# Kernel optimization log

Hardware: AMD Instinct MI355X
Metric: run time of the kernel (lower is better)

## Reference

```python
import jax, jax.numpy as jnp
import numpy as np

B, S, C = 64, 512, 512   # batch, subseq_length, in_features
H, D = 4, 128            # n_heads, hidden_features (H*D == C)
LN_EPS = 1e-5


def setup_inputs() -> dict:
    key = jax.random.key(0)
    k_h, k_w, k_b = jax.random.split(key, 3)
    h = jax.random.normal(k_h, (B, S, C), dtype=jnp.float32)
    # stacked per-head Linear weights, stored as [H, in, hid] for x @ W
    W = jax.random.normal(k_w, (H, C, D), dtype=jnp.float32) * (1.0 / np.sqrt(C))
    b = jax.random.normal(k_b, (H, D), dtype=jnp.float32) * 0.01
    adj = jnp.ones((S, S), dtype=jnp.float32)
    gamma = jnp.ones((C,), dtype=jnp.float32)
    beta = jnp.zeros((C,), dtype=jnp.float32)
    return {"t": 0, "h": h, "W": W, "b": b, "adj": adj, "gamma": gamma, "beta": beta}


def reference(t, h, W, b, adj, gamma, beta):
    # per-head projection: [H, B, S, D]
    hp = jnp.einsum("bsc,hcd->hbsd", h, W) + b[:, None, None, :]
    # raw scores, multiplicative adjacency mask (non-standard: mask BEFORE softmax by multiply)
    scores = jnp.einsum("hbsd,hbtd->hbst", hp, hp) * adj
    attn = jax.nn.softmax(scores, axis=-1)
    out = jnp.einsum("hbst,hbtd->hbsd", attn, hp)
    # concat heads along feature dim -> [B, S, H*D] == [B, S, C]
    out = jnp.transpose(out, (1, 2, 0, 3)).reshape(h.shape[0], h.shape[1], -1)
    # LayerNorm over last dim
    mu = jnp.mean(out, axis=-1, keepdims=True)
    var = jnp.mean(jnp.square(out - mu), axis=-1, keepdims=True)
    out = (out - mu) * jax.lax.rsqrt(var + LN_EPS) * gamma + beta
    # GELU (exact erf form, matching torch nn.GELU default)
    return jax.nn.gelu(out, approximate=False)
```

## Files before the change

kernel.cpp:

```cpp
#include <hip/hip_runtime.h>
#include <stdint.h>


typedef float  f32x4   __attribute__((ext_vector_type(4)));
typedef short  bf16x8  __attribute__((ext_vector_type(8)));
typedef unsigned short ushort8 __attribute__((ext_vector_type(8)));
typedef unsigned int   uint2v  __attribute__((ext_vector_type(2)));

#define GLD16(src, dst)                                                        \
  __builtin_amdgcn_global_load_lds(                                            \
      (const __attribute__((address_space(1))) void*)(src),                    \
      (__attribute__((address_space(3))) void*)(dst), 16, 0, 0)

__device__ __forceinline__ unsigned short f32_to_bf16(float x) {
  union { float f; unsigned int u; } v; v.f = x;
  unsigned int r = v.u + 0x7FFFu + ((v.u >> 16) & 1u);
  return (unsigned short)(r >> 16);
}
__device__ __forceinline__ float bf16_to_f32(unsigned int h) {
  union { float f; unsigned int u; } v; v.u = h << 16;
  return v.f;
}
__device__ __forceinline__ f32x4 mfma16(bf16x8 a, bf16x8 b, f32x4 c) {
  return __builtin_amdgcn_mfma_f32_16x16x32_bf16(a, b, c, 0, 0, 0);
}
__device__ __forceinline__ float bperm_f(int srcLane, float v) {
  return __int_as_float(__builtin_amdgcn_ds_bpermute(srcLane << 2, __float_as_int(v)));
}
__device__ __forceinline__ uint2v tr_read(const unsigned short* p) {
  uint2v r;
  asm volatile("ds_read_b64_tr_b16 %0, %1"
               : "=v"(r)
               : "v"((const __attribute__((address_space(3))) void*)p)
               : "memory");
  return r;
}

__global__ __launch_bounds__(256) void cast_split_h(
    const float* __restrict__ src, unsigned short* __restrict__ dhi,
    unsigned short* __restrict__ dlo) {
  size_t i = ((size_t)blockIdx.x * 256 + threadIdx.x) * 8;
  f32x4 a = *(const f32x4*)(src + i);
  f32x4 b = *(const f32x4*)(src + i + 4);
  ushort8 hi, lo;
#pragma unroll
  for (int e = 0; e < 4; ++e) {
    unsigned short h0 = f32_to_bf16(a[e]);
    hi[e] = h0; lo[e] = f32_to_bf16(a[e] - bf16_to_f32(h0));
    unsigned short h1 = f32_to_bf16(b[e]);
    hi[4 + e] = h1; lo[4 + e] = f32_to_bf16(b[e] - bf16_to_f32(h1));
  }
  *(ushort8*)(dhi + i) = hi;
  *(ushort8*)(dlo + i) = lo;
}

__global__ __launch_bounds__(256) void cast_split_Wt(
    const float* __restrict__ W, unsigned short* __restrict__ whi,
    unsigned short* __restrict__ wlo) {
  int o = blockIdx.x * 256 + threadIdx.x;
  int hd = o >> 16;
  int rem = o & 65535;
  int d = rem >> 9;
  int c = rem & 511;
  float v = W[((size_t)(hd * 512 + c)) * 128 + d];
  unsigned short h0 = f32_to_bf16(v);
  whi[o] = h0;
  wlo[o] = f32_to_bf16(v - bf16_to_f32(h0));
}

__global__ __launch_bounds__(256) void cast_adj(
    const float* __restrict__ src, unsigned short* __restrict__ dst) {
  size_t i = ((size_t)blockIdx.x * 256 + threadIdx.x) * 8;
  f32x4 a = *(const f32x4*)(src + i);
  f32x4 b = *(const f32x4*)(src + i + 4);
  ushort8 o;
#pragma unroll
  for (int e = 0; e < 4; ++e) {
    o[e] = f32_to_bf16(a[e]);
    o[4 + e] = f32_to_bf16(b[e]);
  }
  *(ushort8*)(dst + i) = o;
}

__global__ __launch_bounds__(256, 2) void proj_gemm(
    const unsigned short* __restrict__ ahi, const unsigned short* __restrict__ alo,
    const unsigned short* __restrict__ whi, const unsigned short* __restrict__ wlo,
    const float* __restrict__ bias, unsigned short* __restrict__ hp_hi,
    unsigned short* __restrict__ hp_lo) {
  int bid = blockIdx.x;
  int swz = (bid & 7) * 128 + (bid >> 3);
  int nt = swz & 3, mt = swz >> 2;
  int m0 = mt * 128, n0 = nt * 128;

  __shared__ alignas(16) unsigned short Ah[128 * 32], Al[128 * 32];
  __shared__ alignas(16) unsigned short Bh[128 * 32], Bl[128 * 32];

  int tid = threadIdx.x, wv = tid >> 6, lane = tid & 63;
  int l15 = lane & 15, l4 = lane >> 4;
  int wr = wv >> 1, wc = wv & 1;

  f32x4 acc[4][4];
#pragma unroll
  for (int a = 0; a < 4; ++a)
#pragma unroll
    for (int b = 0; b < 4; ++b) acc[a][b] = (f32x4){0.f, 0.f, 0.f, 0.f};

  for (int ks = 0; ks < 16; ++ks) {
    int k0 = ks * 32;
    for (int i = wv; i < 32; i += 4) {
      int grp = i >> 3, j = i & 7;
      int row = j * 16 + (lane >> 2);
      int off = (lane & 3) * 16;
      int sw = ((row >> 1) & 3) << 4;
      const unsigned short* sb;
      unsigned short* db;
      size_t srcoff;
      if (grp == 0)      { sb = ahi; db = Ah; srcoff = ((size_t)(m0 + row) * 512 + k0) * 2; }
      else if (grp == 1) { sb = alo; db = Al; srcoff = ((size_t)(m0 + row) * 512 + k0) * 2; }
      else if (grp == 2) { sb = whi; db = Bh; srcoff = ((size_t)(nt * 128 + row) * 512 + k0) * 2; }
      else               { sb = wlo; db = Bl; srcoff = ((size_t)(nt * 128 + row) * 512 + k0) * 2; }
      GLD16((const char*)sb + srcoff + (off ^ sw), db + j * 512);
    }
    __syncthreads();

    bf16x8 fah[4], fal[4], fbh[4], fbl[4];
#pragma unroll
    for (int f = 0; f < 4; ++f) {
      int mr = wr * 64 + f * 16 + l15;
      int aadr = mr * 64 + ((16 * l4) ^ (((mr >> 1) & 3) << 4));
      fah[f] = *(const bf16x8*)((const char*)Ah + aadr);
      fal[f] = *(const bf16x8*)((const char*)Al + aadr);
      int nr = wc * 64 + f * 16 + l15;
      int badr = nr * 64 + ((16 * l4) ^ (((nr >> 1) & 3) << 4));
      fbh[f] = *(const bf16x8*)((const char*)Bh + badr);
      fbl[f] = *(const bf16x8*)((const char*)Bl + badr);
    }
#pragma unroll
    for (int a = 0; a < 4; ++a)
#pragma unroll
      for (int b = 0; b < 4; ++b) {
        acc[a][b] = mfma16(fah[a], fbh[b], acc[a][b]);
        acc[a][b] = mfma16(fah[a], fbl[b], acc[a][b]);
        acc[a][b] = mfma16(fal[a], fbh[b], acc[a][b]);
      }
    __syncthreads();
  }

#pragma unroll
  for (int a = 0; a < 4; ++a) {
    __syncthreads();
#pragma unroll
    for (int b = 0; b < 4; ++b) {
      int cloc = wc * 64 + b * 16 + l15;
      float bv = bias[n0 + cloc];
#pragma unroll
      for (int r = 0; r < 4; ++r) {
        int rloc = wr * 16 + 4 * l4 + r;
        float v = acc[a][b][r] + bv;
        unsigned short hh = f32_to_bf16(v);
        Ah[rloc * 128 + cloc] = hh;
        Al[rloc * 128 + cloc] = f32_to_bf16(v - bf16_to_f32(hh));
      }
    }
    __syncthreads();
    int rr = tid >> 3, c16 = (tid & 7) * 16;
    int mg = m0 + (rr >> 4) * 64 + a * 16 + (rr & 15);
    bf16x8 vh0 = *(const bf16x8*)(Ah + rr * 128 + c16);
    bf16x8 vh1 = *(const bf16x8*)(Ah + rr * 128 + c16 + 8);
    bf16x8 vl0 = *(const bf16x8*)(Al + rr * 128 + c16);
    bf16x8 vl1 = *(const bf16x8*)(Al + rr * 128 + c16 + 8);
    *(bf16x8*)(hp_hi + (size_t)mg * 512 + n0 + c16) = vh0;
    *(bf16x8*)(hp_hi + (size_t)mg * 512 + n0 + c16 + 8) = vh1;
    *(bf16x8*)(hp_lo + (size_t)mg * 512 + n0 + c16) = vl0;
    *(bf16x8*)(hp_lo + (size_t)mg * 512 + n0 + c16 + 8) = vl1;
  }
}

__global__ __launch_bounds__(256, 3) void attn_kernel(
    const unsigned short* __restrict__ hp_hi, const unsigned short* __restrict__ hp_lo,
    const unsigned short* __restrict__ adjb, float* __restrict__ out) {
  int bid = blockIdx.x;
  int swz = (bid & 7) * 256 + (bid >> 3);
  int qt = swz & 7;
  int hd = (swz >> 3) & 3;
  int bb = swz >> 5;
  int q0 = qt * 64;

  __shared__ alignas(16) unsigned short SM[24576];

  int tid = threadIdx.x, w = tid >> 6, lane = tid & 63;
  int l15 = lane & 15, l4 = lane >> 4;
  int qg = q0 + w * 16 + l15;

  bf16x8 qh[4], ql[4];
  {
    size_t base = ((size_t)bb * 512 + qg) * 512 + hd * 128 + 8 * l4;
#pragma unroll
    for (int ds = 0; ds < 4; ++ds) {
      qh[ds] = *(const bf16x8*)(hp_hi + base + ds * 32);
      ql[ds] = *(const bf16x8*)(hp_lo + base + ds * 32);
    }
  }

  f32x4 o[8];
#pragma unroll
  for (int vf = 0; vf < 8; ++vf) o[vf] = (f32x4){0.f, 0.f, 0.f, 0.f};
  float m_run = -3.0e38f, l_run = 0.f;

  const unsigned short* ssb = (w & 2) ? hp_lo : hp_hi;
  int sdst = (w & 2) ? 4096 : 0;
  int sdbase = (w & 1) * 4;
  int skv = lane >> 1, sdh = lane & 1;

  {
    size_t rowb = ((size_t)(bb * 512 + skv)) * 1024 + hd * 256 + sdh * 16;
#pragma unroll
    for (int s2 = 0; s2 < 4; ++s2) {
      int sd = sdbase + s2;
      GLD16((const char*)ssb + rowb + sd * 32, SM + sdst + sd * 512);
    }
  }
  asm volatile("s_waitcnt vmcnt(0)" ::: "memory");
  __syncthreads();

  for (int t = 0; t < 16; ++t) {
    int kv0 = t * 32;
    const unsigned short* Kb = SM + ((t & 1) << 13);
    const unsigned short* Khi = Kb;
    const unsigned short* Klo = Kb + 4096;

    if (t < 15) {
      unsigned short* Nb = SM + (((t + 1) & 1) << 13) + sdst;
      size_t rowb = ((size_t)(bb * 512 + kv0 + 32 + skv)) * 1024 + hd * 256 + sdh * 16;
#pragma unroll
      for (int s2 = 0; s2 < 4; ++s2) {
        int sd = sdbase + s2;
        GLD16((const char*)ssb + rowb + sd * 32, Nb + sd * 512);
      }
    }
    uint2 ua0 = *(const uint2*)(adjb + (size_t)qg * 512 + kv0 + 4 * l4);
    uint2 ua1 = *(const uint2*)(adjb + (size_t)qg * 512 + kv0 + 16 + 4 * l4);
    f32x4 av0, av1;
    av0[0] = bf16_to_f32(ua0.x & 0xFFFFu); av0[1] = bf16_to_f32(ua0.x >> 16);
    av0[2] = bf16_to_f32(ua0.y & 0xFFFFu); av0[3] = bf16_to_f32(ua0.y >> 16);
    av1[0] = bf16_to_f32(ua1.x & 0xFFFFu); av1[1] = bf16_to_f32(ua1.x >> 16);
    av1[2] = bf16_to_f32(ua1.y & 0xFFFFu); av1[3] = bf16_to_f32(ua1.y >> 16);

    f32x4 sc0 = {0.f, 0.f, 0.f, 0.f}, sc1 = {0.f, 0.f, 0.f, 0.f};
#pragma unroll
    for (int ds = 0; ds < 4; ++ds) {
      int boff = (2 * ds + (l4 >> 1)) * 1024 + 16 * (l4 & 1);
      int a0 = boff + l15 * 32;
      int a1 = boff + (16 + l15) * 32;
      bf16x8 kh0 = *(const bf16x8*)((const char*)Khi + a0);
      bf16x8 kl0 = *(const bf16x8*)((const char*)Klo + a0);
      bf16x8 kh1 = *(const bf16x8*)((const char*)Khi + a1);
      bf16x8 kl1 = *(const bf16x8*)((const char*)Klo + a1);
      sc0 = mfma16(kh0, qh[ds], sc0); sc1 = mfma16(kh1, qh[ds], sc1);
      sc0 = mfma16(kh0, ql[ds], sc0); sc1 = mfma16(kh1, ql[ds], sc1);
      sc0 = mfma16(kl0, qh[ds], sc0); sc1 = mfma16(kl1, qh[ds], sc1);
    }

    float p0[4], p1[4];
    float tm = -3.0e38f;
#pragma unroll
    for (int r = 0; r < 4; ++r) {
      p0[r] = sc0[r] * av0[r];
      p1[r] = sc1[r] * av1[r];
      tm = fmaxf(tm, fmaxf(p0[r], p1[r]));
    }
    tm = fmaxf(tm, __shfl_xor(tm, 16));
    tm = fmaxf(tm, __shfl_xor(tm, 32));
    if (__any(tm > m_run + 8.0f)) {
      float mn = fmaxf(m_run, tm);
      float scl = __expf(m_run - mn);
      m_run = mn;
      l_run *= scl;
      f32x4 s4;
#pragma unroll
      for (int r = 0; r < 4; ++r) s4[r] = bperm_f(4 * l4 + r, scl);
#pragma unroll
      for (int vf = 0; vf < 8; ++vf)
#pragma unroll
        for (int r = 0; r < 4; ++r) o[vf][r] *= s4[r];
    }
    float ps = 0.f;
#pragma unroll
    for (int r = 0; r < 4; ++r) {
      p0[r] = __expf(p0[r] - m_run); ps += p0[r];
      p1[r] = __expf(p1[r] - m_run); ps += p1[r];
    }
    ps += __shfl_xor(ps, 16);
    ps += __shfl_xor(ps, 32);
    l_run += ps;

    union PU { bf16x8 v; unsigned u[4]; } pah;
#pragma unroll
    for (int i = 0; i < 4; ++i) {
      float fa = (i < 2) ? p0[2 * i] : p1[2 * (i - 2)];
      float fb = (i < 2) ? p0[2 * i + 1] : p1[2 * (i - 2) + 1];
      pah.u[i] = (__float_as_uint(fa) >> 16) |
                 (__float_as_uint(fb) & 0xFFFF0000u);
    }

    const unsigned short* trb = Khi + lane * 4;
    union VU { bf16x8 v; uint2v u2[2]; } vh[8];
#pragma unroll
    for (int vf = 0; vf < 8; ++vf) {
      vh[vf].u2[0] = tr_read(trb + vf * 512);
      vh[vf].u2[1] = tr_read(trb + vf * 512 + 256);
    }
    asm volatile("s_waitcnt lgkmcnt(0)" ::: "memory");
    __builtin_amdgcn_sched_barrier(0);
#pragma unroll
    for (int vf = 0; vf < 8; ++vf)
      o[vf] = mfma16(pah.v, vh[vf].v, o[vf]);
    asm volatile("s_waitcnt vmcnt(0) lgkmcnt(0)" ::: "memory");
    __syncthreads();
  }

  float rinv = 1.0f / l_run;
  f32x4 r4;
#pragma unroll
  for (int r = 0; r < 4; ++r) r4[r] = bperm_f(4 * l4 + r, rinv);
  float* wbase = (float*)SM + w * 2048;
#pragma unroll
  for (int vf = 0; vf < 8; ++vf)
#pragma unroll
    for (int r = 0; r < 4; ++r)
      wbase[(4 * l4 + r) * 128 + vf * 16 + l15] = o[vf][r] * r4[r];
  __syncthreads();
#pragma unroll
  for (int p = 0; p < 4; ++p) {
    int row = p * 4 + l4;
    f32x4 v0 = *(const f32x4*)(wbase + row * 128 + l15 * 8);
    f32x4 v1 = *(const f32x4*)(wbase + row * 128 + l15 * 8 + 4);
    size_t mg = (size_t)bb * 512 + q0 + w * 16 + row;
    float* op = out + mg * 512 + hd * 128 + l15 * 8;
    *(f32x4*)op = v0;
    *(f32x4*)(op + 4) = v1;
  }
}

__global__ __launch_bounds__(256) void ln_gelu_kernel(
    float* __restrict__ io, const float* __restrict__ gamma,
    const float* __restrict__ beta) {
  int w = threadIdx.x >> 6, lane = threadIdx.x & 63;
  size_t row = (size_t)blockIdx.x * 4 + w;
  float* p = io + row * 512;
  f32x4 x0 = *(const f32x4*)(p + lane * 8);
  f32x4 x1 = *(const f32x4*)(p + lane * 8 + 4);
  float s = x0[0] + x0[1] + x0[2] + x0[3] + x1[0] + x1[1] + x1[2] + x1[3];
#pragma unroll
  for (int off = 32; off >= 1; off >>= 1) s += __shfl_xor(s, off);
  float mu = s * (1.0f / 512.0f);
  float vs = 0.f;
#pragma unroll
  for (int e = 0; e < 4; ++e) {
    float d0 = x0[e] - mu; vs += d0 * d0;
    float d1 = x1[e] - mu; vs += d1 * d1;
  }
#pragma unroll
  for (int off = 32; off >= 1; off >>= 1) vs += __shfl_xor(vs, off);
  float rs = rsqrtf(vs * (1.0f / 512.0f) + 1e-5f);
  f32x4 g0 = *(const f32x4*)(gamma + lane * 8);
  f32x4 g1 = *(const f32x4*)(gamma + lane * 8 + 4);
  f32x4 b0 = *(const f32x4*)(beta + lane * 8);
  f32x4 b1 = *(const f32x4*)(beta + lane * 8 + 4);
  f32x4 y0, y1;
#pragma unroll
  for (int e = 0; e < 4; ++e) {
    float y = (x0[e] - mu) * rs * g0[e] + b0[e];
    y0[e] = 0.5f * y * (1.0f + erff(y * 0.70710678118654752f));
    float z = (x1[e] - mu) * rs * g1[e] + b1[e];
    y1[e] = 0.5f * z * (1.0f + erff(z * 0.70710678118654752f));
  }
  *(f32x4*)(p + lane * 8) = y0;
  *(f32x4*)(p + lane * 8 + 4) = y1;
}

extern "C" void kernel_launch(void* const* d_in, const int* in_sizes, int n_in,
                              void* d_out, int out_size, void* d_ws, size_t ws_size,
                              hipStream_t stream) {
  const float* h     = (const float*)d_in[1];
  const float* W     = (const float*)d_in[2];
  const float* bias  = (const float*)d_in[3];
  const float* adj   = (const float*)d_in[4];
  const float* gamma = (const float*)d_in[5];
  const float* beta  = (const float*)d_in[6];
  float* out = (float*)d_out;

  unsigned short* ws = (unsigned short*)d_ws;
  unsigned short* h_hi   = ws;
  unsigned short* h_lo   = ws + 16777216;
  unsigned short* hp_hi  = ws + 33554432;
  unsigned short* hp_lo  = ws + 50331648;
  unsigned short* Wt_hi  = ws + 67108864;
  unsigned short* Wt_lo  = ws + 67371008;
  unsigned short* adj_bf = ws;

  cast_split_h<<<8192, 256, 0, stream>>>(h, h_hi, h_lo);
  cast_split_Wt<<<1024, 256, 0, stream>>>(W, Wt_hi, Wt_lo);
  proj_gemm<<<1024, 256, 0, stream>>>(h_hi, h_lo, Wt_hi, Wt_lo, bias, hp_hi, hp_lo);
  cast_adj<<<128, 256, 0, stream>>>(adj, adj_bf);
  attn_kernel<<<2048, 256, 0, stream>>>(hp_hi, hp_lo, adj_bf, out);
  ln_gelu_kernel<<<8192, 256, 0, stream>>>(out, gamma, beta);
}
```

Baseline: 211.7 us.

## Process two query fragments per wave in attention kernel with 128-thread blocks

Each attention block now runs two waves instead of four, and each wave handles 32 query rows as two 16-row fragments. The K/V tile loaded from shared memory is reused across both fragments, halving LDS reads per MFMA. Each wave now loads twice as much of the K tile into LDS, and the output staging uses a padded 132-float stride. The cost is higher register pressure (doubled accumulators and Q fragments) and fewer waves per block, which may reduce latency hiding.

```diff
diff --git a/kernel.cpp b/kernel.cpp
--- a/kernel.cpp
+++ b/kernel.cpp
@@ -176,7 +176,7 @@
   }
 }
 
-__global__ __launch_bounds__(256, 3) void attn_kernel(
+__global__ __launch_bounds__(128, 2) void attn_kernel(
     const unsigned short* __restrict__ hp_hi, const unsigned short* __restrict__ hp_lo,
     const unsigned short* __restrict__ adjb, float* __restrict__ out) {
   int bid = blockIdx.x;
@@ -186,39 +186,40 @@
   int bb = swz >> 5;
   int q0 = qt * 64;
 
-  __shared__ alignas(16) unsigned short SM[24576];
+  __shared__ alignas(16) unsigned short SM[26624];
 
   int tid = threadIdx.x, w = tid >> 6, lane = tid & 63;
   int l15 = lane & 15, l4 = lane >> 4;
-  int qg = q0 + w * 16 + l15;
-
-  bf16x8 qh[4], ql[4];
-  {
-    size_t base = ((size_t)bb * 512 + qg) * 512 + hd * 128 + 8 * l4;
+  int qgb = q0 + w * 32 + l15;
+
+  bf16x8 qh[2][4], ql[2][4];
+#pragma unroll
+  for (int nf = 0; nf < 2; ++nf) {
+    size_t base = ((size_t)bb * 512 + qgb + nf * 16) * 512 + hd * 128 + 8 * l4;
 #pragma unroll
     for (int ds = 0; ds < 4; ++ds) {
-      qh[ds] = *(const bf16x8*)(hp_hi + base + ds * 32);
-      ql[ds] = *(const bf16x8*)(hp_lo + base + ds * 32);
-    }
-  }
-
-  f32x4 o[8];
-#pragma unroll
-  for (int vf = 0; vf < 8; ++vf) o[vf] = (f32x4){0.f, 0.f, 0.f, 0.f};
-  float m_run = -3.0e38f, l_run = 0.f;
-
-  const unsigned short* ssb = (w & 2) ? hp_lo : hp_hi;
-  int sdst = (w & 2) ? 4096 : 0;
-  int sdbase = (w & 1) * 4;
+      qh[nf][ds] = *(const bf16x8*)(hp_hi + base + ds * 32);
+      ql[nf][ds] = *(const bf16x8*)(hp_lo + base + ds * 32);
+    }
+  }
+
+  f32x4 o[2][8];
+#pragma unroll
+  for (int nf = 0; nf < 2; ++nf)
+#pragma unroll
+    for (int vf = 0; vf < 8; ++vf) o[nf][vf] = (f32x4){0.f, 0.f, 0.f, 0.f};
+  float m_run[2] = {-3.0e38f, -3.0e38f};
+  float l_run[2] = {0.f, 0.f};
+
+  const unsigned short* ssb = w ? hp_lo : hp_hi;
+  int sdst = w ? 4096 : 0;
   int skv = lane >> 1, sdh = lane & 1;
 
   {
     size_t rowb = ((size_t)(bb * 512 + skv)) * 1024 + hd * 256 + sdh * 16;
 #pragma unroll
-    for (int s2 = 0; s2 < 4; ++s2) {
-      int sd = sdbase + s2;
+    for (int sd = 0; sd < 8; ++sd)
       GLD16((const char*)ssb + rowb + sd * 32, SM + sdst + sd * 512);
-    }
   }
   asm volatile("s_waitcnt vmcnt(0)" ::: "memory");
   __syncthreads();
@@ -233,20 +234,22 @@
       unsigned short* Nb = SM + (((t + 1) & 1) << 13) + sdst;
       size_t rowb = ((size_t)(bb * 512 + kv0 + 32 + skv)) * 1024 + hd * 256 + sdh * 16;
 #pragma unroll
-      for (int s2 = 0; s2 < 4; ++s2) {
-        int sd = sdbase + s2;
+      for (int sd = 0; sd < 8; ++sd)
         GLD16((const char*)ssb + rowb + sd * 32, Nb + sd * 512);
-      }
-    }
-    uint2 ua0 = *(const uint2*)(adjb + (size_t)qg * 512 + kv0 + 4 * l4);
-    uint2 ua1 = *(const uint2*)(adjb + (size_t)qg * 512 + kv0 + 16 + 4 * l4);
-    f32x4 av0, av1;
-    av0[0] = bf16_to_f32(ua0.x & 0xFFFFu); av0[1] = bf16_to_f32(ua0.x >> 16);
-    av0[2] = bf16_to_f32(ua0.y & 0xFFFFu); av0[3] = bf16_to_f32(ua0.y >> 16);
-    av1[0] = bf16_to_f32(ua1.x & 0xFFFFu); av1[1] = bf16_to_f32(ua1.x >> 16);
-    av1[2] = bf16_to_f32(ua1.y & 0xFFFFu); av1[3] = bf16_to_f32(ua1.y >> 16);
-
-    f32x4 sc0 = {0.f, 0.f, 0.f, 0.f}, sc1 = {0.f, 0.f, 0.f, 0.f};
+    }
+    uint2 ua[2][2];
+#pragma unroll
+    for (int nf = 0; nf < 2; ++nf) {
+      const unsigned short* ab = adjb + (size_t)(qgb + nf * 16) * 512 + kv0;
+      ua[nf][0] = *(const uint2*)(ab + 4 * l4);
+      ua[nf][1] = *(const uint2*)(ab + 16 + 4 * l4);
+    }
+
+    f32x4 sc[2][2];
+#pragma unroll
+    for (int nf = 0; nf < 2; ++nf)
+#pragma unroll
+      for (int mf = 0; mf < 2; ++mf) sc[nf][mf] = (f32x4){0.f, 0.f, 0.f, 0.f};
 #pragma unroll
     for (int ds = 0; ds < 4; ++ds) {
       int boff = (2 * ds + (l4 >> 1)) * 1024 + 16 * (l4 & 1);
@@ -256,51 +259,68 @@
       bf16x8 kl0 = *(const bf16x8*)((const char*)Klo + a0);
       bf16x8 kh1 = *(const bf16x8*)((const char*)Khi + a1);
       bf16x8 kl1 = *(const bf16x8*)((const char*)Klo + a1);
-      sc0 = mfma16(kh0, qh[ds], sc0); sc1 = mfma16(kh1, qh[ds], sc1);
-      sc0 = mfma16(kh0, ql[ds], sc0); sc1 = mfma16(kh1, ql[ds], sc1);
-      sc0 = mfma16(kl0, qh[ds], sc0); sc1 = mfma16(kl1, qh[ds], sc1);
-    }
-
-    float p0[4], p1[4];
-    float tm = -3.0e38f;
-#pragma unroll
-    for (int r = 0; r < 4; ++r) {
-      p0[r] = sc0[r] * av0[r];
-      p1[r] = sc1[r] * av1[r];
-      tm = fmaxf(tm, fmaxf(p0[r], p1[r]));
-    }
-    tm = fmaxf(tm, __shfl_xor(tm, 16));
-    tm = fmaxf(tm, __shfl_xor(tm, 32));
-    if (__any(tm > m_run + 8.0f)) {
-      float mn = fmaxf(m_run, tm);
-      float scl = __expf(m_run - mn);
-      m_run = mn;
-      l_run *= scl;
-      f32x4 s4;
-#pragma unroll
-      for (int r = 0; r < 4; ++r) s4[r] = bperm_f(4 * l4 + r, scl);
-#pragma unroll
-      for (int vf = 0; vf < 8; ++vf)
-#pragma unroll
-        for (int r = 0; r < 4; ++r) o[vf][r] *= s4[r];
-    }
-    float ps = 0.f;
-#pragma unroll
-    for (int r = 0; r < 4; ++r) {
-      p0[r] = __expf(p0[r] - m_run); ps += p0[r];
-      p1[r] = __expf(p1[r] - m_run); ps += p1[r];
-    }
-    ps += __shfl_xor(ps, 16);
-    ps += __shfl_xor(ps, 32);
-    l_run += ps;
-
-    union PU { bf16x8 v; unsigned u[4]; } pah;
-#pragma unroll
-    for (int i = 0; i < 4; ++i) {
-      float fa = (i < 2) ? p0[2 * i] : p1[2 * (i - 2)];
-      float fb = (i < 2) ? p0[2 * i + 1] : p1[2 * (i - 2) + 1];
-      pah.u[i] = (__float_as_uint(fa) >> 16) |
-                 (__float_as_uint(fb) & 0xFFFF0000u);
+#pragma unroll
+      for (int nf = 0; nf < 2; ++nf) {
+        sc[nf][0] = mfma16(kh0, qh[nf][ds], sc[nf][0]);
+        sc[nf][1] = mfma16(kh1, qh[nf][ds], sc[nf][1]);
+        sc[nf][0] = mfma16(kh0, ql[nf][ds], sc[nf][0]);
+        sc[nf][1] = mfma16(kh1, ql[nf][ds], sc[nf][1]);
+        sc[nf][0] = mfma16(kl0, qh[nf][ds], sc[nf][0]);
+        sc[nf][1] = mfma16(kl1, qh[nf][ds], sc[nf][1]);
+      }
+    }
+
+    union PU { bf16x8 v; unsigned u[4]; } pah[2];
+#pragma unroll
+    for (int nf = 0; nf < 2; ++nf) {
+      f32x4 av0, av1;
+      av0[0] = bf16_to_f32(ua[nf][0].x & 0xFFFFu);
+      av0[1] = bf16_to_f32(ua[nf][0].x >> 16);
+      av0[2] = bf16_to_f32(ua[nf][0].y & 0xFFFFu);
+      av0[3] = bf16_to_f32(ua[nf][0].y >> 16);
+      av1[0] = bf16_to_f32(ua[nf][1].x & 0xFFFFu);
+      av1[1] = bf16_to_f32(ua[nf][1].x >> 16);
+      av1[2] = bf16_to_f32(ua[nf][1].y & 0xFFFFu);
+      av1[3] = bf16_to_f32(ua[nf][1].y >> 16);
+      float p0[4], p1[4];
+      float tm = -3.0e38f;
+#pragma unroll
+      for (int r = 0; r < 4; ++r) {
+        p0[r] = sc[nf][0][r] * av0[r];
+        p1[r] = sc[nf][1][r] * av1[r];
+        tm = fmaxf(tm, fmaxf(p0[r], p1[r]));
+      }
+      tm = fmaxf(tm, __shfl_xor(tm, 16));
+      tm = fmaxf(tm, __shfl_xor(tm, 32));
+      if (__any(tm > m_run[nf] + 8.0f)) {
+        float mn = fmaxf(m_run[nf], tm);
+        float scl = __expf(m_run[nf] - mn);
+        m_run[nf] = mn;
+        l_run[nf] *= scl;
+        f32x4 s4;
+#pragma unroll
+        for (int r = 0; r < 4; ++r) s4[r] = bperm_f(4 * l4 + r, scl);
+#pragma unroll
+        for (int vf = 0; vf < 8; ++vf)
+#pragma unroll
+          for (int r = 0; r < 4; ++r) o[nf][vf][r] *= s4[r];
+      }
+      float ps = 0.f;
+#pragma unroll
+      for (int r = 0; r < 4; ++r) {
+        p0[r] = __expf(p0[r] - m_run[nf]); ps += p0[r];
+        p1[r] = __expf(p1[r] - m_run[nf]); ps += p1[r];
+      }
+      ps += __shfl_xor(ps, 16);
+      ps += __shfl_xor(ps, 32);
+      l_run[nf] += ps;
+#pragma unroll
+      for (int i = 0; i < 4; ++i) {
+        float fa = (i < 2) ? p0[2 * i] : p1[2 * (i - 2)];
+        float fb = (i < 2) ? p0[2 * i + 1] : p1[2 * (i - 2) + 1];
+        pah[nf].u[i] = (__float_as_uint(fa) >> 16) |
+                       (__float_as_uint(fb) & 0xFFFF0000u);
+      }
     }
 
     const unsigned short* trb = Khi + lane * 4;
@@ -313,30 +333,40 @@
     asm volatile("s_waitcnt lgkmcnt(0)" ::: "memory");
     __builtin_amdgcn_sched_barrier(0);
 #pragma unroll
-    for (int vf = 0; vf < 8; ++vf)
-      o[vf] = mfma16(pah.v, vh[vf].v, o[vf]);
+    for (int vf = 0; vf < 8; ++vf) {
+      o[0][vf] = mfma16(pah[0].v, vh[vf].v, o[0][vf]);
+      o[1][vf] = mfma16(pah[1].v, vh[vf].v, o[1][vf]);
+    }
     asm volatile("s_waitcnt vmcnt(0) lgkmcnt(0)" ::: "memory");
     __syncthreads();
   }
 
-  float rinv = 1.0f / l_run;
-  f32x4 r4;
-#pragma unroll
-  for (int r = 0; r < 4; ++r) r4[r] = bperm_f(4 * l4 + r, rinv);
-  float* wbase = (float*)SM + w * 2048;
+  float rinv0 = 1.0f / l_run[0];
+  float rinv1 = 1.0f / l_run[1];
+  f32x4 r40, r41;
+#pragma unroll
+  for (int r = 0; r < 4; ++r) {
+    r40[r] = bperm_f(4 * l4 + r, rinv0);
+    r41[r] = bperm_f(4 * l4 + r, rinv1);
+  }
+  float* wb = (float*)SM;
 #pragma unroll
   for (int vf = 0; vf < 8; ++vf)
 #pragma unroll
-    for (int r = 0; r < 4; ++r)
-      wbase[(4 * l4 + r) * 128 + vf * 16 + l15] = o[vf][r] * r4[r];
+    for (int r = 0; r < 4; ++r) {
+      int c = vf * 16 + l15;
+      wb[(w * 32 + 4 * l4 + r) * 132 + c]      = o[0][vf][r] * r40[r];
+      wb[(w * 32 + 16 + 4 * l4 + r) * 132 + c] = o[1][vf][r] * r41[r];
+    }
   __syncthreads();
 #pragma unroll
-  for (int p = 0; p < 4; ++p) {
-    int row = p * 4 + l4;
-    f32x4 v0 = *(const f32x4*)(wbase + row * 128 + l15 * 8);
-    f32x4 v1 = *(const f32x4*)(wbase + row * 128 + l15 * 8 + 4);
-    size_t mg = (size_t)bb * 512 + q0 + w * 16 + row;
-    float* op = out + mg * 512 + hd * 128 + l15 * 8;
+  for (int p = 0; p < 8; ++p) {
+    int row = p * 8 + (tid >> 4);
+    int col = (tid & 15) * 8;
+    f32x4 v0 = *(const f32x4*)(wb + row * 132 + col);
+    f32x4 v1 = *(const f32x4*)(wb + row * 132 + col + 4);
+    size_t mg = (size_t)bb * 512 + q0 + row;
+    float* op = out + mg * 512 + hd * 128 + col;
     *(f32x4*)op = v0;
     *(f32x4*)(op + 4) = v1;
   }
@@ -403,6 +433,6 @@
   cast_split_Wt<<<1024, 256, 0, stream>>>(W, Wt_hi, Wt_lo);
   proj_gemm<<<1024, 256, 0, stream>>>(h_hi, h_lo, Wt_hi, Wt_lo, bias, hp_hi, hp_lo);
   cast_adj<<<128, 256, 0, stream>>>(adj, adj_bf);
-  attn_kernel<<<2048, 256, 0, stream>>>(hp_hi, hp_lo, adj_bf, out);
+  attn_kernel<<<2048, 128, 0, stream>>>(hp_hi, hp_lo, adj_bf, out);
   ln_gelu_kernel<<<8192, 256, 0, stream>>>(out, gamma, beta);
 }
```

Measured after the change: 232.1 us. 1.1x slower.

## Double-buffer projection GEMM loads and store attention output as bf16

Applied to the files above, without the earlier changes.

The projection GEMM now uses a two-stage LDS buffer. The next K-slice is prefetched with global_load_lds while MFMAs run on the current slice, which hides global load latency behind compute. Separately, the attention kernel writes its output as bf16 to a workspace buffer instead of fp32, and the LayerNorm+GELU kernel reads bf16 and writes fp32 to the final output. This halves the intermediate traffic at some precision cost before LayerNorm. The doubled LDS (64KB) may lower GEMM occupancy.

```diff
diff --git a/kernel.cpp b/kernel.cpp
--- a/kernel.cpp
+++ b/kernel.cpp
@@ -92,8 +92,7 @@
   int nt = swz & 3, mt = swz >> 2;
   int m0 = mt * 128, n0 = nt * 128;
 
-  __shared__ alignas(16) unsigned short Ah[128 * 32], Al[128 * 32];
-  __shared__ alignas(16) unsigned short Bh[128 * 32], Bl[128 * 32];
+  __shared__ alignas(16) unsigned short PSM[32768];
 
   int tid = threadIdx.x, wv = tid >> 6, lane = tid & 63;
   int l15 = lane & 15, l4 = lane >> 4;
@@ -105,24 +104,42 @@
 #pragma unroll
     for (int b = 0; b < 4; ++b) acc[a][b] = (f32x4){0.f, 0.f, 0.f, 0.f};
 
+  for (int i = wv; i < 32; i += 4) {
+    int grp = i >> 3, j = i & 7;
+    int row = j * 16 + (lane >> 2);
+    int off = (lane & 3) * 16;
+    int sw = ((row >> 1) & 3) << 4;
+    const unsigned short* sb = (grp == 0) ? ahi : (grp == 1) ? alo
+                             : (grp == 2) ? whi : wlo;
+    size_t srcoff = (grp < 2) ? ((size_t)(m0 + row) * 512) * 2
+                              : ((size_t)(nt * 128 + row) * 512) * 2;
+    GLD16((const char*)sb + srcoff + (off ^ sw), PSM + grp * 4096 + j * 512);
+  }
+  asm volatile("s_waitcnt vmcnt(0)" ::: "memory");
+  __syncthreads();
+
   for (int ks = 0; ks < 16; ++ks) {
-    int k0 = ks * 32;
-    for (int i = wv; i < 32; i += 4) {
-      int grp = i >> 3, j = i & 7;
-      int row = j * 16 + (lane >> 2);
-      int off = (lane & 3) * 16;
-      int sw = ((row >> 1) & 3) << 4;
-      const unsigned short* sb;
-      unsigned short* db;
-      size_t srcoff;
-      if (grp == 0)      { sb = ahi; db = Ah; srcoff = ((size_t)(m0 + row) * 512 + k0) * 2; }
-      else if (grp == 1) { sb = alo; db = Al; srcoff = ((size_t)(m0 + row) * 512 + k0) * 2; }
-      else if (grp == 2) { sb = whi; db = Bh; srcoff = ((size_t)(nt * 128 + row) * 512 + k0) * 2; }
-      else               { sb = wlo; db = Bl; srcoff = ((size_t)(nt * 128 + row) * 512 + k0) * 2; }
-      GLD16((const char*)sb + srcoff + (off ^ sw), db + j * 512);
-    }
-    __syncthreads();
-
+    const unsigned short* base = PSM + (ks & 1) * 16384;
+    if (ks < 15) {
+      unsigned short* nb = PSM + ((ks + 1) & 1) * 16384;
+      int k1 = (ks + 1) * 32;
+      for (int i = wv; i < 32; i += 4) {
+        int grp = i >> 3, j = i & 7;
+        int row = j * 16 + (lane >> 2);
+        int off = (lane & 3) * 16;
+        int sw = ((row >> 1) & 3) << 4;
+        const unsigned short* sb = (grp == 0) ? ahi : (grp == 1) ? alo
+                                 : (grp == 2) ? whi : wlo;
+        size_t srcoff = (grp < 2) ? ((size_t)(m0 + row) * 512 + k1) * 2
+                                  : ((size_t)(nt * 128 + row) * 512 + k1) * 2;
+        GLD16((const char*)sb + srcoff + (off ^ sw), nb + grp * 4096 + j * 512);
+      }
+    }
+
+    const unsigned short* Ah = base;
+    const unsigned short* Al = base + 4096;
+    const unsigned short* Bh = base + 8192;
+    const unsigned short* Bl = base + 12288;
     bf16x8 fah[4], fal[4], fbh[4], fbl[4];
 #pragma unroll
     for (int f = 0; f < 4; ++f) {
@@ -143,9 +160,12 @@
         acc[a][b] = mfma16(fah[a], fbl[b], acc[a][b]);
         acc[a][b] = mfma16(fal[a], fbh[b], acc[a][b]);
       }
+    asm volatile("s_waitcnt vmcnt(0) lgkmcnt(0)" ::: "memory");
     __syncthreads();
   }
 
+  unsigned short* Eh = PSM;
+  unsigned short* El = PSM + 4096;
 #pragma unroll
   for (int a = 0; a < 4; ++a) {
     __syncthreads();
@@ -158,17 +178,17 @@
         int rloc = wr * 16 + 4 * l4 + r;
         float v = acc[a][b][r] + bv;
         unsigned short hh = f32_to_bf16(v);
-        Ah[rloc * 128 + cloc] = hh;
-        Al[rloc * 128 + cloc] = f32_to_bf16(v - bf16_to_f32(hh));
+        Eh[rloc * 128 + cloc] = hh;
+        El[rloc * 128 + cloc] = f32_to_bf16(v - bf16_to_f32(hh));
       }
     }
     __syncthreads();
     int rr = tid >> 3, c16 = (tid & 7) * 16;
     int mg = m0 + (rr >> 4) * 64 + a * 16 + (rr & 15);
-    bf16x8 vh0 = *(const bf16x8*)(Ah + rr * 128 + c16);
-    bf16x8 vh1 = *(const bf16x8*)(Ah + rr * 128 + c16 + 8);
-    bf16x8 vl0 = *(const bf16x8*)(Al + rr * 128 + c16);
-    bf16x8 vl1 = *(const bf16x8*)(Al + rr * 128 + c16 + 8);
+    bf16x8 vh0 = *(const bf16x8*)(Eh + rr * 128 + c16);
+    bf16x8 vh1 = *(const bf16x8*)(Eh + rr * 128 + c16 + 8);
+    bf16x8 vl0 = *(const bf16x8*)(El + rr * 128 + c16);
+    bf16x8 vl1 = *(const bf16x8*)(El + rr * 128 + c16 + 8);
     *(bf16x8*)(hp_hi + (size_t)mg * 512 + n0 + c16) = vh0;
     *(bf16x8*)(hp_hi + (size_t)mg * 512 + n0 + c16 + 8) = vh1;
     *(bf16x8*)(hp_lo + (size_t)mg * 512 + n0 + c16) = vl0;
@@ -178,7 +198,7 @@
 
 __global__ __launch_bounds__(256, 3) void attn_kernel(
     const unsigned short* __restrict__ hp_hi, const unsigned short* __restrict__ hp_lo,
-    const unsigned short* __restrict__ adjb, float* __restrict__ out) {
+    const unsigned short* __restrict__ adjb, unsigned short* __restrict__ ob) {
   int bid = blockIdx.x;
   int swz = (bid & 7) * 256 + (bid >> 3);
   int qt = swz & 7;
@@ -335,30 +355,36 @@
     int row = p * 4 + l4;
     f32x4 v0 = *(const f32x4*)(wbase + row * 128 + l15 * 8);
     f32x4 v1 = *(const f32x4*)(wbase + row * 128 + l15 * 8 + 4);
+    ushort8 o8;
+#pragma unroll
+    for (int e = 0; e < 4; ++e) {
+      o8[e] = f32_to_bf16(v0[e]);
+      o8[4 + e] = f32_to_bf16(v1[e]);
+    }
     size_t mg = (size_t)bb * 512 + q0 + w * 16 + row;
-    float* op = out + mg * 512 + hd * 128 + l15 * 8;
-    *(f32x4*)op = v0;
-    *(f32x4*)(op + 4) = v1;
+    *(ushort8*)(ob + mg * 512 + hd * 128 + l15 * 8) = o8;
   }
 }
 
 __global__ __launch_bounds__(256) void ln_gelu_kernel(
-    float* __restrict__ io, const float* __restrict__ gamma,
-    const float* __restrict__ beta) {
+    const unsigned short* __restrict__ in, float* __restrict__ outp,
+    const float* __restrict__ gamma, const float* __restrict__ beta) {
   int w = threadIdx.x >> 6, lane = threadIdx.x & 63;
   size_t row = (size_t)blockIdx.x * 4 + w;
-  float* p = io + row * 512;
-  f32x4 x0 = *(const f32x4*)(p + lane * 8);
-  f32x4 x1 = *(const f32x4*)(p + lane * 8 + 4);
-  float s = x0[0] + x0[1] + x0[2] + x0[3] + x1[0] + x1[1] + x1[2] + x1[3];
+  ushort8 v = *(const ushort8*)(in + row * 512 + lane * 8);
+  float x[8];
+#pragma unroll
+  for (int e = 0; e < 8; ++e) x[e] = bf16_to_f32((unsigned int)(unsigned short)v[e]);
+  float s = 0.f;
+#pragma unroll
+  for (int e = 0; e < 8; ++e) s += x[e];
 #pragma unroll
   for (int off = 32; off >= 1; off >>= 1) s += __shfl_xor(s, off);
   float mu = s * (1.0f / 512.0f);
   float vs = 0.f;
 #pragma unroll
-  for (int e = 0; e < 4; ++e) {
-    float d0 = x0[e] - mu; vs += d0 * d0;
-    float d1 = x1[e] - mu; vs += d1 * d1;
+  for (int e = 0; e < 8; ++e) {
+    float d = x[e] - mu; vs += d * d;
   }
 #pragma unroll
   for (int off = 32; off >= 1; off >>= 1) vs += __shfl_xor(vs, off);
@@ -370,13 +396,14 @@
   f32x4 y0, y1;
 #pragma unroll
   for (int e = 0; e < 4; ++e) {
-    float y = (x0[e] - mu) * rs * g0[e] + b0[e];
+    float y = (x[e] - mu) * rs * g0[e] + b0[e];
     y0[e] = 0.5f * y * (1.0f + erff(y * 0.70710678118654752f));
-    float z = (x1[e] - mu) * rs * g1[e] + b1[e];
+    float z = (x[4 + e] - mu) * rs * g1[e] + b1[e];
     y1[e] = 0.5f * z * (1.0f + erff(z * 0.70710678118654752f));
   }
-  *(f32x4*)(p + lane * 8) = y0;
-  *(f32x4*)(p + lane * 8 + 4) = y1;
+  float* p = outp + row * 512 + lane * 8;
+  *(f32x4*)p = y0;
+  *(f32x4*)(p + 4) = y1;
 }
 
 extern "C" void kernel_launch(void* const* d_in, const int* in_sizes, int n_in,
@@ -398,11 +425,12 @@
   unsigned short* Wt_hi  = ws + 67108864;
   unsigned short* Wt_lo  = ws + 67371008;
   unsigned short* adj_bf = ws;
+  unsigned short* ob     = ws + 16777216;
 
   cast_split_h<<<8192, 256, 0, stream>>>(h, h_hi, h_lo);
   cast_split_Wt<<<1024, 256, 0, stream>>>(W, Wt_hi, Wt_lo);
   proj_gemm<<<1024, 256, 0, stream>>>(h_hi, h_lo, Wt_hi, Wt_lo, bias, hp_hi, hp_lo);
   cast_adj<<<128, 256, 0, stream>>>(adj, adj_bf);
-  attn_kernel<<<2048, 256, 0, stream>>>(hp_hi, hp_lo, adj_bf, out);
-  ln_gelu_kernel<<<8192, 256, 0, stream>>>(out, gamma, beta);
-}
+  attn_kernel<<<2048, 256, 0, stream>>>(hp_hi, hp_lo, adj_bf, ob);
+  ln_gelu_kernel<<<8192, 256, 0, stream>>>(ob, out, gamma, beta);
+}
```

After: 216.0 us. 1.02x slower.
